# Kernel tuning notes

Hardware: AMD Instinct MI355X
Metric: run time of the kernel (lower is better)

The kernel has to match this reference:

```python
import jax, jax.numpy as jnp
import numpy as np

NUM_NODES = 100000
NUM_EDGES = 1600000
HID = 128
NODE_DIM = 5
MSG_DIM = 2


def _mlp(x, params):
    # 3 hidden ReLU layers + linear head, matching nn.Sequential in torch
    (W0, b0, W1, b1, W2, b2, W3, b3) = params
    h = jax.nn.relu(x @ W0 + b0)
    h = jax.nn.relu(h @ W1 + b1)
    h = jax.nn.relu(h @ W2 + b2)
    return h @ W3 + b3


def setup_inputs() -> dict:
    key = jax.random.key(0)
    ks = jax.random.split(key, 12)
    nodes = jax.random.normal(ks[0], (NUM_NODES, NODE_DIM), dtype=jnp.float32)
    edge_index = jax.random.randint(ks[1], (2, NUM_EDGES), 0, NUM_NODES, dtype=jnp.int32)

    def lin(k, fan_in, fan_out):
        # kaiming-uniform-ish init, scale irrelevant for correctness baseline
        bound = 1.0 / np.sqrt(fan_in)
        return jax.random.uniform(k, (fan_in, fan_out), jnp.float32, -bound, bound)

    return {
        "nodes": nodes,
        "edge_index": edge_index,
        "Wm0": lin(ks[2], 2 * NODE_DIM, HID), "bm0": jnp.zeros((HID,), jnp.float32),
        "Wm1": lin(ks[3], HID, HID),          "bm1": jnp.zeros((HID,), jnp.float32),
        "Wm2": lin(ks[4], HID, HID),          "bm2": jnp.zeros((HID,), jnp.float32),
        "Wm3": lin(ks[5], HID, MSG_DIM),      "bm3": jnp.zeros((MSG_DIM,), jnp.float32),
        "Wu0": lin(ks[6], NODE_DIM + MSG_DIM, HID), "bu0": jnp.zeros((HID,), jnp.float32),
        "Wu1": lin(ks[7], HID, HID),          "bu1": jnp.zeros((HID,), jnp.float32),
        "Wu2": lin(ks[8], HID, HID),          "bu2": jnp.zeros((HID,), jnp.float32),
        "Wu3": lin(ks[9], HID, MSG_DIM),      "bu3": jnp.zeros((MSG_DIM,), jnp.float32),
    }


def reference(nodes, edge_index, Wm0, bm0, Wm1, bm1, Wm2, bm2, Wm3, bm3,
              Wu0, bu0, Wu1, bu1, Wu2, bu2, Wu3, bu3):
    senders = edge_index[0]
    receivers = edge_index[1]
    # gather endpoints: [E, 2*node_dim]
    edge_inputs = jnp.concatenate([nodes[senders], nodes[receivers]], axis=-1)
    messages = _mlp(edge_inputs, (Wm0, bm0, Wm1, bm1, Wm2, bm2, Wm3, bm3))  # [E, msg_dim]
    # scatter-add pooling rho_{e->v}
    pooled = jax.ops.segment_sum(messages, receivers, num_segments=nodes.shape[0])  # [N, msg_dim]
    node_update_input = jnp.concatenate([nodes, pooled], axis=-1)  # [N, node_dim+msg_dim]
    delta_v = _mlp(node_update_input, (Wu0, bu0, Wu1, bu1, Wu2, bu2, Wu3, bu3))  # [N, 2]
    # Euler step on velocity columns 2:4
    updated = jnp.concatenate([nodes[:, :2], nodes[:, 2:4] + delta_v, nodes[:, 4:]], axis=-1)
    return updated
```

## Files before the change

### kernel.cpp

```cpp
#include <hip/hip_runtime.h>
#include <hip/hip_bf16.h>

#define NE 1600000
#define NN 100000
#define PSCALE 131072.0f

typedef __attribute__((ext_vector_type(8))) short s16x8;
typedef __attribute__((ext_vector_type(4))) float f32x4;
typedef __attribute__((ext_vector_type(16))) float f32x16;
typedef __attribute__((ext_vector_type(4))) int i32x4;
typedef __attribute__((ext_vector_type(4))) uint u32x4;

__device__ __forceinline__ ushort f2b(float v) {
  union { __hip_bfloat16 h; ushort u; } c; c.h = __float2bfloat16(v); return c.u;
}
__device__ __forceinline__ uint cvtpk(float a, float b) {
  uint r;
  asm("v_cvt_pk_bf16_f32 %0, %1, %2" : "=v"(r) : "v"(a), "v"(b));
  return r;
}
__device__ __forceinline__ uint pkrelu(float a, float b) {
  a = fmaxf(a, 0.f); b = fmaxf(b, 0.f);
  return cvtpk(a, b);
}
__device__ __forceinline__ f32x16 mfma32(s16x8 a, s16x8 b, f32x16 c) {
  return __builtin_amdgcn_mfma_f32_32x32x16_bf16(a, b, c, 0, 0, 0);
}
__device__ __forceinline__ u32x4 packg(const f32x16& a, int g) {
  u32x4 r;
#pragma unroll
  for (int w = 0; w < 4; w++) r[w] = pkrelu(a[8 * g + 2 * w], a[8 * g + 2 * w + 1]);
  return r;
}
__device__ __forceinline__ f32x16 loadbias(const float* bias, int mt, int hi) {
  f32x16 b;
#pragma unroll
  for (int q4 = 0; q4 < 4; q4++) {
    f32x4 v = *(const f32x4*)(bias + mt * 32 + q4 * 8 + hi * 4);
#pragma unroll
    for (int i = 0; i < 4; i++) b[q4 * 4 + i] = v[i];
  }
  return b;
}

__global__ void prep_weights(const float* s0, const float* s1, const float* s2, const float* s3,
                             const float* s4, const float* s5, const float* s6, const float* s7,
                             const float* bm0, const float* bu0, ushort* dst) {
  const int NFRAG[8] = {4, 32, 32, 8, 4, 32, 32, 8};
  const int offs[8]  = {0, 2048, 18432, 34816, 38912, 40960, 57344, 73728};
  const float* srcs[8] = {s0, s1, s2, s3, s4, s5, s6, s7};
  int b = blockIdx.x;
  int cnt = NFRAG[b] * 512;
  const float* src = srcs[b];
  bool isProducer = (b == 0 || b == 4);
  bool isHead = (b == 3 || b == 7);
  int F1 = (b < 4) ? 5 : 2;
  int kbias = (b < 4) ? 13 : 10;
  const float* bp = (b < 4) ? bm0 : bu0;
  ushort* d = dst + offs[b];
  for (int idx = threadIdx.x; idx < cnt; idx += blockDim.x) {
    int f = idx >> 9, r = idx & 511, lane = r >> 3, j = r & 7;
    int hi = lane >> 5, m = lane & 31;
    float v = 0.f;
    if (isProducer) {
      int ch = f * 32 + m;
      int k = hi * 8 + j;
      int row = -1;
      if (k < 5) row = k;
      else if (k >= 8 && k < 8 + F1) row = k - 3;
      if (row >= 0) v = src[row * 128 + ch];
      else if (k == kbias) v = bp[ch];
    } else {
      int s = isHead ? f : (f >> 2);
      int k = s * 16 + hi * 8 + j;
      int c = (k & ~12) | ((k & 4) << 1) | ((k & 8) >> 1);
      if (isHead) v = (m < 2) ? src[c * 2 + m] : 0.f;
      else {
        int ch = (f & 3) * 32 + m;
        v = src[c * 128 + ch];
      }
    }
    d[idx] = f2b(v);
  }
}

template <int MODE>
__global__ __launch_bounds__(512, 2)
void gnn_kernel(const float* __restrict__ nodes,
                const int* __restrict__ eidx,
                unsigned long long* __restrict__ pooled,
                const ushort* __restrict__ wsrc,
                const float* __restrict__ b1g, const float* __restrict__ b2g,
                const float* __restrict__ b3g,
                float* __restrict__ out) {
  __shared__ __align__(16) ushort wlds[38912];
  __shared__ __align__(16) float bias1[128];
  __shared__ __align__(16) float bias2[128];
  __shared__ __align__(16) float bias3[16];
  {
    i32x4* dw = (i32x4*)wlds;
    const i32x4* sw = (const i32x4*)wsrc;
    for (int i = threadIdx.x; i < 4864; i += 512) dw[i] = sw[i];
    if (threadIdx.x < 128) {
      bias1[threadIdx.x] = b1g[threadIdx.x];
      bias2[threadIdx.x] = b2g[threadIdx.x];
    }
    if (threadIdx.x < 16) bias3[threadIdx.x] = (threadIdx.x < 2) ? b3g[threadIdx.x] : 0.f;
  }
  __syncthreads();

  const int wv = threadIdx.x >> 6;
  const int l = threadIdx.x & 63;
  const int hi = l >> 5;
  const int e32 = l & 31;
  auto LF = [&](int base, int f) {
    return *(const s16x8*)(wlds + base + f * 512 + l * 8);
  };

  int wid = blockIdx.x * 8 + wv;
  int nwv = gridDim.x * 8;
  const int NB = (MODE == 0) ? (NE / 32) : (NN / 32);
  const f32x16 z16 = {0.f, 0.f, 0.f, 0.f, 0.f, 0.f, 0.f, 0.f,
                      0.f, 0.f, 0.f, 0.f, 0.f, 0.f, 0.f, 0.f};

  float g0 = 0, g1 = 0, g2 = 0, g3 = 0, g4 = 0;
  auto PREF = [&](int bb) {
    if (bb < NB) {
      int e = (bb << 5) + e32;
      if (MODE == 0) {
        int idx = eidx[hi * NE + e];
        const float* np_ = nodes + idx * 5;
        g0 = np_[0]; g1 = np_[1]; g2 = np_[2]; g3 = np_[3]; g4 = np_[4];
      } else {
        if (hi == 0) {
          const float* np_ = nodes + e * 5;
          g0 = np_[0]; g1 = np_[1]; g2 = np_[2]; g3 = np_[3]; g4 = np_[4];
        } else {
          unsigned long long pl = pooled[e];
          int x32 = (int)(uint)pl;
          int y32 = (int)(pl >> 32) + (x32 < 0 ? 1 : 0);
          g0 = (float)x32 * (1.f / PSCALE);
          g1 = (float)y32 * (1.f / PSCALE);
        }
      }
    }
  };
  PREF(wid);

#pragma unroll 1
  for (int b = wid; b < NB; b += nwv) {
    const int rbase = b << 5;
    int rc = 0;
    if (MODE == 0) rc = eidx[NE + rbase + e32];
    s16x8 xf;
    {
      u32x4 f = {0u, 0u, 0u, 0u};
      if (MODE == 0) {
        f[0] = cvtpk(g0, g1); f[1] = cvtpk(g2, g3);
        f[2] = cvtpk(g4, hi ? 1.0f : 0.0f);
      } else {
        if (hi == 0) { f[0] = cvtpk(g0, g1); f[1] = cvtpk(g2, g3); f[2] = cvtpk(g4, 0.f); }
        else         { f[0] = cvtpk(g0, g1); f[1] = cvtpk(1.0f, 0.f); }
      }
      xf = __builtin_bit_cast(s16x8, f);
    }
    PREF(b + nwv);

    s16x8 w0f0 = LF(0, 0), w0f1 = LF(0, 1), w0f2 = LF(0, 2), w0f3 = LF(0, 3);
    s16x8 wf[2][8];
#pragma unroll
    for (int s = 0; s < 8; s++) wf[0][s] = LF(2048, s * 4);

    u32x4 phA[4][2];
    {
      f32x16 a;
      a = mfma32(w0f0, xf, z16); phA[0][0] = packg(a, 0); phA[0][1] = packg(a, 1);
      a = mfma32(w0f1, xf, z16); phA[1][0] = packg(a, 0); phA[1][1] = packg(a, 1);
      a = mfma32(w0f2, xf, z16); phA[2][0] = packg(a, 0); phA[2][1] = packg(a, 1);
      a = mfma32(w0f3, xf, z16); phA[3][0] = packg(a, 0); phA[3][1] = packg(a, 1);
    }
    u32x4 phB[4][2];
#pragma unroll
    for (int mt = 0; mt < 4; mt++) {
      if (mt < 3) {
#pragma unroll
        for (int s = 0; s < 8; s++) wf[(mt + 1) & 1][s] = LF(2048, s * 4 + mt + 1);
      } else {
#pragma unroll
        for (int s = 0; s < 8; s++) wf[(mt + 1) & 1][s] = LF(18432, s * 4);
      }
      f32x16 a = loadbias(bias1, mt, hi);
#pragma unroll
      for (int s = 0; s < 8; s++)
        a = mfma32(wf[mt & 1][s], __builtin_bit_cast(s16x8, phA[s >> 1][s & 1]), a);
      phB[mt][0] = packg(a, 0);
      phB[mt][1] = packg(a, 1);
    }
    u32x4 phC[4][2];
#pragma unroll
    for (int mt = 0; mt < 4; mt++) {
      if (mt < 3) {
#pragma unroll
        for (int s = 0; s < 8; s++) wf[(mt + 1) & 1][s] = LF(18432, s * 4 + mt + 1);
      } else {
#pragma unroll
        for (int s = 0; s < 8; s++) wf[(mt + 1) & 1][s] = LF(34816, s);
      }
      f32x16 a = loadbias(bias2, mt, hi);
#pragma unroll
      for (int s = 0; s < 8; s++)
        a = mfma32(wf[mt & 1][s], __builtin_bit_cast(s16x8, phB[s >> 1][s & 1]), a);
      phC[mt][0] = packg(a, 0);
      phC[mt][1] = packg(a, 1);
    }
    f32x16 a = mfma32(wf[0][0], __builtin_bit_cast(s16x8, phC[0][0]), z16);
#pragma unroll
    for (int s = 1; s < 8; s++)
      a = mfma32(wf[0][s], __builtin_bit_cast(s16x8, phC[s >> 1][s & 1]), a);

    int e = rbase + e32;
    if (hi == 0) {
      float mv0 = a[0] + bias3[0], mv1 = a[1] + bias3[1];
      if (MODE == 0) {
        int ix = (int)rintf(mv0 * PSCALE);
        int iy = (int)rintf(mv1 * PSCALE);
        long long ad = (((long long)iy) << 32) + (long long)ix;
        atomicAdd(&pooled[rc], (unsigned long long)ad);
      } else {
        out[e * 5 + 2] = nodes[e * 5 + 2] + mv0;
        out[e * 5 + 3] = nodes[e * 5 + 3] + mv1;
      }
    } else if (MODE == 1) {
      out[e * 5 + 0] = nodes[e * 5 + 0];
      out[e * 5 + 1] = nodes[e * 5 + 1];
      out[e * 5 + 4] = nodes[e * 5 + 4];
    }
  }
}

extern "C" void kernel_launch(void* const* d_in, const int* in_sizes, int n_in,
                              void* d_out, int out_size, void* d_ws, size_t ws_size,
                              hipStream_t stream) {
  const float* nodes = (const float*)d_in[0];
  const int* eidx = (const int*)d_in[1];
  const float* Wm0 = (const float*)d_in[2];  const float* bm0 = (const float*)d_in[3];
  const float* Wm1 = (const float*)d_in[4];  const float* bm1 = (const float*)d_in[5];
  const float* Wm2 = (const float*)d_in[6];  const float* bm2 = (const float*)d_in[7];
  const float* Wm3 = (const float*)d_in[8];  const float* bm3 = (const float*)d_in[9];
  const float* Wu0 = (const float*)d_in[10]; const float* bu0 = (const float*)d_in[11];
  const float* Wu1 = (const float*)d_in[12]; const float* bu1 = (const float*)d_in[13];
  const float* Wu2 = (const float*)d_in[14]; const float* bu2 = (const float*)d_in[15];
  const float* Wu3 = (const float*)d_in[16]; const float* bu3 = (const float*)d_in[17];

  unsigned long long* pooled = (unsigned long long*)d_ws;
  ushort* wbuf = (ushort*)((char*)d_ws + 800000);

  hipMemsetAsync(pooled, 0, NN * 8, stream);
  prep_weights<<<8, 256, 0, stream>>>(Wm0, Wm1, Wm2, Wm3, Wu0, Wu1, Wu2, Wu3,
                                      bm0, bu0, wbuf);

  gnn_kernel<0><<<256, 512, 0, stream>>>(nodes, eidx, pooled, wbuf,
                                         bm1, bm2, bm3, nullptr);
  gnn_kernel<1><<<256, 512, 0, stream>>>(nodes, nullptr, pooled, wbuf + 38912,
                                         bu1, bu2, bu3, (float*)d_out);
}
```

Before: 165.9 us.

## Process two 32-edge groups per wave to reuse LDS weight fragments

```diff
diff --git a/kernel.cpp b/kernel.cpp
--- a/kernel.cpp
+++ b/kernel.cpp
@@ -119,121 +119,144 @@
 
   int wid = blockIdx.x * 8 + wv;
   int nwv = gridDim.x * 8;
-  const int NB = (MODE == 0) ? (NE / 32) : (NN / 32);
+  const int NB = (MODE == 0) ? (NE / 64) : ((NN + 63) / 64);
   const f32x16 z16 = {0.f, 0.f, 0.f, 0.f, 0.f, 0.f, 0.f, 0.f,
                       0.f, 0.f, 0.f, 0.f, 0.f, 0.f, 0.f, 0.f};
 
-  float g0 = 0, g1 = 0, g2 = 0, g3 = 0, g4 = 0;
+  float g[2][5] = {{0.f, 0.f, 0.f, 0.f, 0.f}, {0.f, 0.f, 0.f, 0.f, 0.f}};
   auto PREF = [&](int bb) {
     if (bb < NB) {
-      int e = (bb << 5) + e32;
+#pragma unroll
+      for (int eg = 0; eg < 2; eg++) {
+        int e = (bb << 6) + (eg << 5) + e32;
+        if (MODE == 0) {
+          int idx = eidx[hi * NE + e];
+          const float* np_ = nodes + idx * 5;
+          g[eg][0] = np_[0]; g[eg][1] = np_[1]; g[eg][2] = np_[2];
+          g[eg][3] = np_[3]; g[eg][4] = np_[4];
+        } else if (e < NN) {
+          if (hi == 0) {
+            const float* np_ = nodes + e * 5;
+            g[eg][0] = np_[0]; g[eg][1] = np_[1]; g[eg][2] = np_[2];
+            g[eg][3] = np_[3]; g[eg][4] = np_[4];
+          } else {
+            unsigned long long pl = pooled[e];
+            int x32 = (int)(uint)pl;
+            int y32 = (int)(pl >> 32) + (x32 < 0 ? 1 : 0);
+            g[eg][0] = (float)x32 * (1.f / PSCALE);
+            g[eg][1] = (float)y32 * (1.f / PSCALE);
+          }
+        }
+      }
+    }
+  };
+  PREF(wid);
+
+#pragma unroll 1
+  for (int b = wid; b < NB; b += nwv) {
+    const int rbase = b << 6;
+    int rc0 = 0, rc1 = 0;
+    if (MODE == 0 && hi == 0) {
+      rc0 = eidx[NE + rbase + e32];
+      rc1 = eidx[NE + rbase + 32 + e32];
+    }
+    s16x8 xf[2];
+#pragma unroll
+    for (int eg = 0; eg < 2; eg++) {
+      u32x4 f = {0u, 0u, 0u, 0u};
       if (MODE == 0) {
-        int idx = eidx[hi * NE + e];
-        const float* np_ = nodes + idx * 5;
-        g0 = np_[0]; g1 = np_[1]; g2 = np_[2]; g3 = np_[3]; g4 = np_[4];
+        f[0] = cvtpk(g[eg][0], g[eg][1]); f[1] = cvtpk(g[eg][2], g[eg][3]);
+        f[2] = cvtpk(g[eg][4], hi ? 1.0f : 0.0f);
       } else {
         if (hi == 0) {
-          const float* np_ = nodes + e * 5;
-          g0 = np_[0]; g1 = np_[1]; g2 = np_[2]; g3 = np_[3]; g4 = np_[4];
+          f[0] = cvtpk(g[eg][0], g[eg][1]); f[1] = cvtpk(g[eg][2], g[eg][3]);
+          f[2] = cvtpk(g[eg][4], 0.f);
         } else {
-          unsigned long long pl = pooled[e];
-          int x32 = (int)(uint)pl;
-          int y32 = (int)(pl >> 32) + (x32 < 0 ? 1 : 0);
-          g0 = (float)x32 * (1.f / PSCALE);
-          g1 = (float)y32 * (1.f / PSCALE);
+          f[0] = cvtpk(g[eg][0], g[eg][1]); f[1] = cvtpk(1.0f, 0.f);
         }
       }
-    }
-  };
-  PREF(wid);
-
-#pragma unroll 1
-  for (int b = wid; b < NB; b += nwv) {
-    const int rbase = b << 5;
-    int rc = 0;
-    if (MODE == 0) rc = eidx[NE + rbase + e32];
-    s16x8 xf;
+      xf[eg] = __builtin_bit_cast(s16x8, f);
+    }
+    PREF(b + nwv);
+
+    u32x4 phA[4][2][2];
     {
-      u32x4 f = {0u, 0u, 0u, 0u};
-      if (MODE == 0) {
-        f[0] = cvtpk(g0, g1); f[1] = cvtpk(g2, g3);
-        f[2] = cvtpk(g4, hi ? 1.0f : 0.0f);
-      } else {
-        if (hi == 0) { f[0] = cvtpk(g0, g1); f[1] = cvtpk(g2, g3); f[2] = cvtpk(g4, 0.f); }
-        else         { f[0] = cvtpk(g0, g1); f[1] = cvtpk(1.0f, 0.f); }
-      }
-      xf = __builtin_bit_cast(s16x8, f);
-    }
-    PREF(b + nwv);
-
-    s16x8 w0f0 = LF(0, 0), w0f1 = LF(0, 1), w0f2 = LF(0, 2), w0f3 = LF(0, 3);
-    s16x8 wf[2][8];
-#pragma unroll
-    for (int s = 0; s < 8; s++) wf[0][s] = LF(2048, s * 4);
-
-    u32x4 phA[4][2];
+      s16x8 w0[4];
+#pragma unroll
+      for (int mt = 0; mt < 4; mt++) w0[mt] = LF(0, mt);
+#pragma unroll
+      for (int mt = 0; mt < 4; mt++) {
+        f32x16 a0 = mfma32(w0[mt], xf[0], z16);
+        f32x16 a1 = mfma32(w0[mt], xf[1], z16);
+        phA[mt][0][0] = packg(a0, 0); phA[mt][1][0] = packg(a0, 1);
+        phA[mt][0][1] = packg(a1, 0); phA[mt][1][1] = packg(a1, 1);
+      }
+    }
+    u32x4 phB[4][2][2];
+#pragma unroll
+    for (int mt = 0; mt < 4; mt++) {
+      s16x8 wf[8];
+#pragma unroll
+      for (int s = 0; s < 8; s++) wf[s] = LF(2048, s * 4 + mt);
+      f32x16 a0 = loadbias(bias1, mt, hi);
+      f32x16 a1 = a0;
+#pragma unroll
+      for (int s = 0; s < 8; s++) {
+        a0 = mfma32(wf[s], __builtin_bit_cast(s16x8, phA[s >> 1][s & 1][0]), a0);
+        a1 = mfma32(wf[s], __builtin_bit_cast(s16x8, phA[s >> 1][s & 1][1]), a1);
+      }
+      phB[mt][0][0] = packg(a0, 0); phB[mt][1][0] = packg(a0, 1);
+      phB[mt][0][1] = packg(a1, 0); phB[mt][1][1] = packg(a1, 1);
+    }
+    u32x4 phC[4][2][2];
+#pragma unroll
+    for (int mt = 0; mt < 4; mt++) {
+      s16x8 wf[8];
+#pragma unroll
+      for (int s = 0; s < 8; s++) wf[s] = LF(18432, s * 4 + mt);
+      f32x16 a0 = loadbias(bias2, mt, hi);
+      f32x16 a1 = a0;
+#pragma unroll
+      for (int s = 0; s < 8; s++) {
+        a0 = mfma32(wf[s], __builtin_bit_cast(s16x8, phB[s >> 1][s & 1][0]), a0);
+        a1 = mfma32(wf[s], __builtin_bit_cast(s16x8, phB[s >> 1][s & 1][1]), a1);
+      }
+      phC[mt][0][0] = packg(a0, 0); phC[mt][1][0] = packg(a0, 1);
+      phC[mt][0][1] = packg(a1, 0); phC[mt][1][1] = packg(a1, 1);
+    }
+    f32x16 ah0, ah1;
     {
-      f32x16 a;
-      a = mfma32(w0f0, xf, z16); phA[0][0] = packg(a, 0); phA[0][1] = packg(a, 1);
-      a = mfma32(w0f1, xf, z16); phA[1][0] = packg(a, 0); phA[1][1] = packg(a, 1);
-      a = mfma32(w0f2, xf, z16); phA[2][0] = packg(a, 0); phA[2][1] = packg(a, 1);
-      a = mfma32(w0f3, xf, z16); phA[3][0] = packg(a, 0); phA[3][1] = packg(a, 1);
-    }
-    u32x4 phB[4][2];
-#pragma unroll
-    for (int mt = 0; mt < 4; mt++) {
-      if (mt < 3) {
-#pragma unroll
-        for (int s = 0; s < 8; s++) wf[(mt + 1) & 1][s] = LF(2048, s * 4 + mt + 1);
-      } else {
-#pragma unroll
-        for (int s = 0; s < 8; s++) wf[(mt + 1) & 1][s] = LF(18432, s * 4);
-      }
-      f32x16 a = loadbias(bias1, mt, hi);
-#pragma unroll
-      for (int s = 0; s < 8; s++)
-        a = mfma32(wf[mt & 1][s], __builtin_bit_cast(s16x8, phA[s >> 1][s & 1]), a);
-      phB[mt][0] = packg(a, 0);
-      phB[mt][1] = packg(a, 1);
-    }
-    u32x4 phC[4][2];
-#pragma unroll
-    for (int mt = 0; mt < 4; mt++) {
-      if (mt < 3) {
-#pragma unroll
-        for (int s = 0; s < 8; s++) wf[(mt + 1) & 1][s] = LF(18432, s * 4 + mt + 1);
-      } else {
-#pragma unroll
-        for (int s = 0; s < 8; s++) wf[(mt + 1) & 1][s] = LF(34816, s);
-      }
-      f32x16 a = loadbias(bias2, mt, hi);
-#pragma unroll
-      for (int s = 0; s < 8; s++)
-        a = mfma32(wf[mt & 1][s], __builtin_bit_cast(s16x8, phB[s >> 1][s & 1]), a);
-      phC[mt][0] = packg(a, 0);
-      phC[mt][1] = packg(a, 1);
-    }
-    f32x16 a = mfma32(wf[0][0], __builtin_bit_cast(s16x8, phC[0][0]), z16);
-#pragma unroll
-    for (int s = 1; s < 8; s++)
-      a = mfma32(wf[0][s], __builtin_bit_cast(s16x8, phC[s >> 1][s & 1]), a);
-
-    int e = rbase + e32;
-    if (hi == 0) {
-      float mv0 = a[0] + bias3[0], mv1 = a[1] + bias3[1];
-      if (MODE == 0) {
-        int ix = (int)rintf(mv0 * PSCALE);
-        int iy = (int)rintf(mv1 * PSCALE);
-        long long ad = (((long long)iy) << 32) + (long long)ix;
-        atomicAdd(&pooled[rc], (unsigned long long)ad);
-      } else {
-        out[e * 5 + 2] = nodes[e * 5 + 2] + mv0;
-        out[e * 5 + 3] = nodes[e * 5 + 3] + mv1;
-      }
-    } else if (MODE == 1) {
-      out[e * 5 + 0] = nodes[e * 5 + 0];
-      out[e * 5 + 1] = nodes[e * 5 + 1];
-      out[e * 5 + 4] = nodes[e * 5 + 4];
+      s16x8 w3[8];
+#pragma unroll
+      for (int s = 0; s < 8; s++) w3[s] = LF(34816, s);
+      ah0 = mfma32(w3[0], __builtin_bit_cast(s16x8, phC[0][0][0]), z16);
+      ah1 = mfma32(w3[0], __builtin_bit_cast(s16x8, phC[0][0][1]), z16);
+#pragma unroll
+      for (int s = 1; s < 8; s++) {
+        ah0 = mfma32(w3[s], __builtin_bit_cast(s16x8, phC[s >> 1][s & 1][0]), ah0);
+        ah1 = mfma32(w3[s], __builtin_bit_cast(s16x8, phC[s >> 1][s & 1][1]), ah1);
+      }
+    }
+#pragma unroll
+    for (int eg = 0; eg < 2; eg++) {
+      int e = rbase + (eg << 5) + e32;
+      const f32x16& a = eg ? ah1 : ah0;
+      if (hi == 0) {
+        float mv0 = a[0] + bias3[0], mv1 = a[1] + bias3[1];
+        if (MODE == 0) {
+          int ix = (int)rintf(mv0 * PSCALE);
+          int iy = (int)rintf(mv1 * PSCALE);
+          long long ad = (((long long)iy) << 32) + (long long)ix;
+          atomicAdd(&pooled[eg ? rc1 : rc0], (unsigned long long)ad);
+        } else if (e < NN) {
+          out[e * 5 + 2] = nodes[e * 5 + 2] + mv0;
+          out[e * 5 + 3] = nodes[e * 5 + 3] + mv1;
+        }
+      } else if (MODE == 1 && e < NN) {
+        out[e * 5 + 0] = nodes[e * 5 + 0];
+        out[e * 5 + 1] = nodes[e * 5 + 1];
+        out[e * 5 + 4] = nodes[e * 5 + 4];
+      }
     }
   }
 }
```

After: 167.1 us. No clear change (+0.7%).

## Software-pipeline layer-0 of next batch and keep layer-0 weights in registers

Applied to the files above, without the earlier changes.

```diff
diff --git a/kernel.cpp b/kernel.cpp
--- a/kernel.cpp
+++ b/kernel.cpp
@@ -85,7 +85,7 @@
 }
 
 template <int MODE>
-__global__ __launch_bounds__(512, 2)
+__global__ __launch_bounds__(512, 1)
 void gnn_kernel(const float* __restrict__ nodes,
                 const int* __restrict__ eidx,
                 unsigned long long* __restrict__ pooled,
@@ -122,6 +122,10 @@
   const int NB = (MODE == 0) ? (NE / 32) : (NN / 32);
   const f32x16 z16 = {0.f, 0.f, 0.f, 0.f, 0.f, 0.f, 0.f, 0.f,
                       0.f, 0.f, 0.f, 0.f, 0.f, 0.f, 0.f, 0.f};
+
+  s16x8 w0p[4];
+#pragma unroll
+  for (int mt = 0; mt < 4; mt++) w0p[mt] = LF(0, mt);
 
   float g0 = 0, g1 = 0, g2 = 0, g3 = 0, g4 = 0;
   auto PREF = [&](int bb) {
@@ -145,82 +149,83 @@
       }
     }
   };
+  s16x8 xf;
+  auto BUILDXF = [&]() {
+    u32x4 f = {0u, 0u, 0u, 0u};
+    if (MODE == 0) {
+      f[0] = cvtpk(g0, g1); f[1] = cvtpk(g2, g3);
+      f[2] = cvtpk(g4, hi ? 1.0f : 0.0f);
+    } else {
+      if (hi == 0) { f[0] = cvtpk(g0, g1); f[1] = cvtpk(g2, g3); f[2] = cvtpk(g4, 0.f); }
+      else         { f[0] = cvtpk(g0, g1); f[1] = cvtpk(1.0f, 0.f); }
+    }
+    xf = __builtin_bit_cast(s16x8, f);
+  };
+  u32x4 phA[4][2];
+  auto L0 = [&]() {
+#pragma unroll
+    for (int mt = 0; mt < 4; mt++) {
+      f32x16 a = mfma32(w0p[mt], xf, z16);
+      phA[mt][0] = packg(a, 0);
+      phA[mt][1] = packg(a, 1);
+    }
+  };
+
   PREF(wid);
+  if (wid < NB) {
+    BUILDXF();
+    PREF(wid + nwv);
+    L0();
+  }
 
 #pragma unroll 1
   for (int b = wid; b < NB; b += nwv) {
     const int rbase = b << 5;
     int rc = 0;
     if (MODE == 0) rc = eidx[NE + rbase + e32];
-    s16x8 xf;
-    {
-      u32x4 f = {0u, 0u, 0u, 0u};
-      if (MODE == 0) {
-        f[0] = cvtpk(g0, g1); f[1] = cvtpk(g2, g3);
-        f[2] = cvtpk(g4, hi ? 1.0f : 0.0f);
-      } else {
-        if (hi == 0) { f[0] = cvtpk(g0, g1); f[1] = cvtpk(g2, g3); f[2] = cvtpk(g4, 0.f); }
-        else         { f[0] = cvtpk(g0, g1); f[1] = cvtpk(1.0f, 0.f); }
-      }
-      xf = __builtin_bit_cast(s16x8, f);
-    }
-    PREF(b + nwv);
-
-    s16x8 w0f0 = LF(0, 0), w0f1 = LF(0, 1), w0f2 = LF(0, 2), w0f3 = LF(0, 3);
-    s16x8 wf[2][8];
-#pragma unroll
-    for (int s = 0; s < 8; s++) wf[0][s] = LF(2048, s * 4);
-
-    u32x4 phA[4][2];
-    {
-      f32x16 a;
-      a = mfma32(w0f0, xf, z16); phA[0][0] = packg(a, 0); phA[0][1] = packg(a, 1);
-      a = mfma32(w0f1, xf, z16); phA[1][0] = packg(a, 0); phA[1][1] = packg(a, 1);
-      a = mfma32(w0f2, xf, z16); phA[2][0] = packg(a, 0); phA[2][1] = packg(a, 1);
-      a = mfma32(w0f3, xf, z16); phA[3][0] = packg(a, 0); phA[3][1] = packg(a, 1);
-    }
     u32x4 phB[4][2];
 #pragma unroll
     for (int mt = 0; mt < 4; mt++) {
-      if (mt < 3) {
-#pragma unroll
-        for (int s = 0; s < 8; s++) wf[(mt + 1) & 1][s] = LF(2048, s * 4 + mt + 1);
-      } else {
-#pragma unroll
-        for (int s = 0; s < 8; s++) wf[(mt + 1) & 1][s] = LF(18432, s * 4);
-      }
+      s16x8 wf[8];
+#pragma unroll
+      for (int s = 0; s < 8; s++) wf[s] = LF(2048, s * 4 + mt);
       f32x16 a = loadbias(bias1, mt, hi);
 #pragma unroll
       for (int s = 0; s < 8; s++)
-        a = mfma32(wf[mt & 1][s], __builtin_bit_cast(s16x8, phA[s >> 1][s & 1]), a);
+        a = mfma32(wf[s], __builtin_bit_cast(s16x8, phA[s >> 1][s & 1]), a);
       phB[mt][0] = packg(a, 0);
       phB[mt][1] = packg(a, 1);
     }
     u32x4 phC[4][2];
 #pragma unroll
     for (int mt = 0; mt < 4; mt++) {
-      if (mt < 3) {
-#pragma unroll
-        for (int s = 0; s < 8; s++) wf[(mt + 1) & 1][s] = LF(18432, s * 4 + mt + 1);
-      } else {
-#pragma unroll
-        for (int s = 0; s < 8; s++) wf[(mt + 1) & 1][s] = LF(34816, s);
-      }
+      s16x8 wf[8];
+#pragma unroll
+      for (int s = 0; s < 8; s++) wf[s] = LF(18432, s * 4 + mt);
       f32x16 a = loadbias(bias2, mt, hi);
 #pragma unroll
       for (int s = 0; s < 8; s++)
-        a = mfma32(wf[mt & 1][s], __builtin_bit_cast(s16x8, phB[s >> 1][s & 1]), a);
+        a = mfma32(wf[s], __builtin_bit_cast(s16x8, phB[s >> 1][s & 1]), a);
       phC[mt][0] = packg(a, 0);
       phC[mt][1] = packg(a, 1);
     }
-    f32x16 a = mfma32(wf[0][0], __builtin_bit_cast(s16x8, phC[0][0]), z16);
+    s16x8 w3[8];
+#pragma unroll
+    for (int s = 0; s < 8; s++) w3[s] = LF(34816, s);
+    int b2 = b + nwv;
+    if (b2 < NB) {
+      BUILDXF();
+      PREF(b2 + nwv);
+      L0();
+    }
+    f32x16 ah = mfma32(w3[0], __builtin_bit_cast(s16x8, phC[0][0]), z16);
 #pragma unroll
     for (int s = 1; s < 8; s++)
-      a = mfma32(wf[0][s], __builtin_bit_cast(s16x8, phC[s >> 1][s & 1]), a);
+      ah = mfma32(w3[s], __builtin_bit_cast(s16x8, phC[s >> 1][s & 1]), ah);
 
     int e = rbase + e32;
     if (hi == 0) {
-      float mv0 = a[0] + bias3[0], mv1 = a[1] + bias3[1];
+      float mv0 = ah[0] + bias3[0], mv1 = ah[1] + bias3[1];
       if (MODE == 0) {
         int ix = (int)rintf(mv0 * PSCALE);
         int iy = (int)rintf(mv1 * PSCALE);
```

Measured after the change: 170.8 us. 3.0% more time.
